# Optimization experiments

Measured on AMD Instinct MI355X. Metric: run time of the kernel, lower is better.

The kernel has to match this reference:

```python
import jax, jax.numpy as jnp
import numpy as np

# Faithful JAX reference for VoxelModule.forward.
# The torch module builds, per batch element, a dict mapping
#   key = vx*10000 + vy*100 + vz  (vx,vy,vz = int(coord * (voxel_size-1)))
# to the list of point indices falling in that voxel.
# Dicts are not jit-able; the equivalent parallel/sort-based grouping is:
#   keys        [B,N] : per-point voxel key (same integer math as torch)
#   order       [B,N] : stable argsort of keys -> point indices grouped by voxel
#   sorted_keys [B,N] : keys in grouped order (run boundaries delimit voxels)
# This (keys, order, sorted_keys) triple encodes exactly the same grouping
# information as the list-of-dicts output.

B = 16
N = 500_000
VOXEL_SIZE = 40  # keys require per-axis index < 100, so voxel_size <= 100


def setup_inputs() -> dict:
    key = jax.random.key(0)
    point_cloud = jax.random.uniform(key, (B, N, 3), dtype=jnp.float32)  # coords in [0,1)
    return {"point_cloud": point_cloud, "voxel_size": VOXEL_SIZE}


def reference(point_cloud, voxel_size):
    # int(x) in Python truncates toward zero; coords are non-negative so
    # truncation == floor. astype(int32) truncates, matching torch code.
    idx = (point_cloud * (voxel_size - 1)).astype(jnp.int32)  # [B,N,3]
    keys = idx[..., 0] * 10000 + idx[..., 1] * 100 + idx[..., 2]  # [B,N]
    # Stable sort: within a voxel, point indices stay in ascending order,
    # matching the append order of the torch dict-building loop.
    order = jnp.argsort(keys, axis=-1, stable=True)  # [B,N] grouped point ids
    sorted_keys = jnp.take_along_axis(keys, order, axis=-1)  # [B,N]
    return keys, order, sorted_keys
```

## Files before the change

### kernel.cpp

```cpp
#include <hip/hip_runtime.h>


#define B 16
#define N 500000
#define BN (B * N)
#define NC2 122
#define RELB 512
#define CAP2 4736
#define TPB1 256
#define NW1 (TPB1 / 64)
#define PPB 2048
#define CPB ((N + PPB - 1) / PPB)
#define NIT4 3

__global__ __launch_bounds__(TPB1, 8) void pass1(const float* __restrict__ pc,
                                                 const int* __restrict__ vs,
                                                 int* __restrict__ keys,
                                                 int* __restrict__ ccnt,
                                                 int* __restrict__ staged) {
    int b = blockIdx.x / CPB;
    int chunk = blockIdx.x % CPB;
    int t = threadIdx.x;
    int w = t >> 6;
    int lane = t & 63;
    __shared__ int lh[NW1][NC2];
    __shared__ int lst[NC2];
    __shared__ int gadj[NC2];
    __shared__ int lim[NC2];
    __shared__ int buf[PPB];
    __shared__ unsigned char cidb[PPB];
    for (int k = lane; k < NC2; k += 64) lh[w][k] = 0;
    float scale = (float)(vs[0] - 1);
    long gb0 = (long)b * N;
    int i0 = chunk * PPB + t * 8;
    int c2v[8], rv[8], pk8[8];
    bool valid = (i0 < N);
    if (valid) {
        const float4* F = (const float4*)(pc + 3 * (gb0 + i0));
        float4 f0 = F[0], f1 = F[1], f2 = F[2], f3 = F[3], f4 = F[4], f5 = F[5];
        float xs[8] = {f0.x, f0.w, f1.z, f2.y, f3.x, f3.w, f4.z, f5.y};
        float ys[8] = {f0.y, f1.x, f1.w, f2.z, f3.y, f4.x, f4.w, f5.z};
        float zs[8] = {f0.z, f1.y, f2.x, f2.w, f3.z, f4.y, f5.x, f5.w};
        int kk[8];
#pragma unroll
        for (int j = 0; j < 8; ++j) {
            int vx = (int)(xs[j] * scale);
            int vy = (int)(ys[j] * scale);
            int vz = (int)(zs[j] * scale);
            kk[j] = vx * 10000 + vy * 100 + vz;
            int lin = (vx * 40 + vy) * 40 + vz;
            int c2 = lin >> 9;
            c2v[j] = c2;
            pk8[j] = ((lin & 511) << 19) | (i0 + j);
            rv[j] = atomicAdd(&lh[w][c2], 1);
        }
        int4 k0; k0.x = kk[0]; k0.y = kk[1]; k0.z = kk[2]; k0.w = kk[3];
        int4 k1; k1.x = kk[4]; k1.y = kk[5]; k1.z = kk[6]; k1.w = kk[7];
        int4* K = (int4*)(keys + gb0 + i0);
        K[0] = k0; K[1] = k1;
    }
    __syncthreads();
    if (t < 64) {
        int idx0 = 2 * t, idx1 = 2 * t + 1;
        int run0 = 0, run1 = 0;
        if (idx0 < NC2) {
#pragma unroll
            for (int ww = 0; ww < NW1; ++ww) { int v = lh[ww][idx0]; lh[ww][idx0] = run0; run0 += v; }
#pragma unroll
            for (int ww = 0; ww < NW1; ++ww) { int v = lh[ww][idx1]; lh[ww][idx1] = run1; run1 += v; }
        }
        int s = run0 + run1;
        int x = s;
#pragma unroll
        for (int d = 1; d < 64; d <<= 1) { int y = __shfl_up(x, d, 64); if (t >= d) x += y; }
        int excl = x - s;
        if (idx0 < NC2) {
            int l0 = excl, l1 = excl + run0;
            lst[idx0] = l0; lst[idx1] = l1;
            int g0 = run0 ? atomicAdd(&ccnt[b * NC2 + idx0], run0) : 0;
            int g1 = run1 ? atomicAdd(&ccnt[b * NC2 + idx1], run1) : 0;
            gadj[idx0] = idx0 * CAP2 + g0 - l0;
            gadj[idx1] = idx1 * CAP2 + g1 - l1;
            lim[idx0] = l0 + CAP2 - g0;
            lim[idx1] = l1 + CAP2 - g1;
        }
    }
    __syncthreads();
    if (valid) {
#pragma unroll
        for (int j = 0; j < 8; ++j) {
            int c2 = c2v[j];
            int pos = lst[c2] + lh[w][c2] + rv[j];
            buf[pos] = pk8[j];
            cidb[pos] = (unsigned char)c2;
        }
    }
    __syncthreads();
    int nval = N - chunk * PPB; if (nval > PPB) nval = PPB;
    long sbase = (long)b * NC2 * CAP2;
#pragma unroll
    for (int q = 0; q < PPB / TPB1; ++q) {
        int p = t + q * TPB1;
        if (p < nval) {
            int e = buf[p];
            int c = cidb[p];
            if (p < lim[c]) staged[sbase + gadj[c] + p] = e;
        }
    }
}

__global__ __launch_bounds__(512) void pass2(const int* __restrict__ ccnt,
                                             const int* __restrict__ staged,
                                             int* __restrict__ order_out,
                                             int* __restrict__ skeys_out) {
    int bc = blockIdx.x;
    int b = bc / NC2;
    int c2 = bc % NC2;
    int t = threadIdx.x;
    __shared__ int h[RELB];
    __shared__ int st[RELB + 1];
    __shared__ int skeyL[RELB];
    __shared__ int srt[CAP2];
    __shared__ int bsh;
    int cnt = ccnt[bc]; if (cnt > CAP2) cnt = CAP2;
    if (cnt == 0) return;

    {
        int z = t;
        h[z] = 0;
        int lin = (c2 << 9) + z;
        int vx = lin / 1600;
        int r = lin - vx * 1600;
        int vy = r / 40;
        int vz = r - vy * 40;
        skeyL[z] = vx * 10000 + vy * 100 + vz;
    }
    if (t < 64) {
        int idx0 = 2 * t, idx1 = 2 * t + 1;
        int v0 = 0, v1 = 0;
        if (idx0 < NC2) {
            v0 = ccnt[b * NC2 + idx0]; if (v0 > CAP2) v0 = CAP2;
            v1 = ccnt[b * NC2 + idx1]; if (v1 > CAP2) v1 = CAP2;
        }
        int s = v0 + v1;
        int x = s;
#pragma unroll
        for (int d = 1; d < 64; d <<= 1) { int y = __shfl_up(x, d, 64); if (t >= d) x += y; }
        int excl = x - s;
        if (idx0 == c2) bsh = excl;
        if (idx1 == c2) bsh = excl + v0;
    }
    __syncthreads();

    long rb = (long)bc * CAP2;
    const int4* reg4 = (const int4*)(staged + rb);
    int n4 = cnt >> 2;
    int4 ev4[NIT4];
#pragma unroll
    for (int q = 0; q < NIT4; ++q) {
        int p4 = t + q * 512;
        if (p4 < n4) {
            int4 e = reg4[p4];
            ev4[q] = e;
            atomicAdd(&h[e.x >> 19], 1);
            atomicAdd(&h[e.y >> 19], 1);
            atomicAdd(&h[e.z >> 19], 1);
            atomicAdd(&h[e.w >> 19], 1);
        }
    }
    int evt = 0; bool tv = false;
    {
        int p = (n4 << 2) + t;
        if (p < cnt) { evt = staged[rb + p]; tv = true; atomicAdd(&h[evt >> 19], 1); }
    }
    __syncthreads();

    if (t < 64) {
        int vals[8]; int s = 0;
#pragma unroll
        for (int j = 0; j < 8; ++j) { int v = h[8 * t + j]; vals[j] = s; s += v; }
        int x = s;
#pragma unroll
        for (int d = 1; d < 64; d <<= 1) { int y = __shfl_up(x, d, 64); if (t >= d) x += y; }
        int excl = x - s;
#pragma unroll
        for (int j = 0; j < 8; ++j) { st[8 * t + j] = excl + vals[j]; h[8 * t + j] = 0; }
        if (t == 63) st[RELB] = x;
    }
    __syncthreads();

#pragma unroll
    for (int q = 0; q < NIT4; ++q) {
        int p4 = t + q * 512;
        if (p4 < n4) {
            int4 e = ev4[q];
            int z0 = e.x >> 19; srt[st[z0] + atomicAdd(&h[z0], 1)] = e.x;
            int z1 = e.y >> 19; srt[st[z1] + atomicAdd(&h[z1], 1)] = e.y;
            int z2 = e.z >> 19; srt[st[z2] + atomicAdd(&h[z2], 1)] = e.z;
            int z3 = e.w >> 19; srt[st[z3] + atomicAdd(&h[z3], 1)] = e.w;
        }
    }
    if (tv) { int z = evt >> 19; srt[st[z] + atomicAdd(&h[z], 1)] = evt; }
    __syncthreads();

    long ob = (long)b * N + bsh;
    for (int p = t; p < cnt; p += 512) {
        int v = srt[p];
        int z = v >> 19;
        int s = st[z], e2 = st[z + 1];
        int rank = 0;
        for (int j = s; j < e2; ++j) rank += (srt[j] < v);
        order_out[ob + s + rank] = v & 0x7FFFF;
        skeys_out[ob + s + rank] = skeyL[z];
    }
}

extern "C" void kernel_launch(void* const* d_in, const int* in_sizes, int n_in,
                              void* d_out, int out_size, void* d_ws, size_t ws_size,
                              hipStream_t stream) {
    const float* pc = (const float*)d_in[0];
    const int* vs = (const int*)d_in[1];
    int* out = (int*)d_out;
    int* keys_out = out;
    int* order_out = out + BN;
    int* skeys_out = out + 2 * BN;

    int* ccnt = (int*)d_ws;
    int* staged = ccnt + B * NC2;

    hipMemsetAsync(ccnt, 0, (size_t)B * NC2 * sizeof(int), stream);
    pass1<<<B * CPB, TPB1, 0, stream>>>(pc, vs, keys_out, ccnt, staged);
    pass2<<<B * NC2, 512, 0, stream>>>(ccnt, staged, order_out, skeys_out);
}
```

Measured before the change: 231.9 us.

## Enlarge pass1 chunks to 8192 points, 16 per thread, nontemporal key stores

Pass1 now runs 512 threads per block, each handling 16 points, so every block bins 8192 points instead of 2048. Larger chunks cut the number of per-block global atomics on the coarse-bucket counters and give longer contiguous scatter runs into the staged buffer. Per-point bucket id and local rank are packed into one register to save registers, and key writes use nontemporal vector stores. The trade-offs are more shared memory and registers per block, fewer resident blocks, and a longer serial scan across 8 warps.

```diff
diff --git a/kernel.cpp b/kernel.cpp
--- a/kernel.cpp
+++ b/kernel.cpp
@@ -7,17 +7,20 @@
 #define NC2 122
 #define RELB 512
 #define CAP2 4736
-#define TPB1 256
+#define TPB1 512
 #define NW1 (TPB1 / 64)
-#define PPB 2048
+#define PPB 8192
+#define PPT 16
 #define CPB ((N + PPB - 1) / PPB)
 #define NIT4 3
 
-__global__ __launch_bounds__(TPB1, 8) void pass1(const float* __restrict__ pc,
-                                                 const int* __restrict__ vs,
-                                                 int* __restrict__ keys,
-                                                 int* __restrict__ ccnt,
-                                                 int* __restrict__ staged) {
+typedef int vint4 __attribute__((ext_vector_type(4)));
+
+__global__ __launch_bounds__(TPB1) void pass1(const float* __restrict__ pc,
+                                              const int* __restrict__ vs,
+                                              int* __restrict__ keys,
+                                              int* __restrict__ ccnt,
+                                              int* __restrict__ staged) {
     int b = blockIdx.x / CPB;
     int chunk = blockIdx.x % CPB;
     int t = threadIdx.x;
@@ -32,32 +35,34 @@
     for (int k = lane; k < NC2; k += 64) lh[w][k] = 0;
     float scale = (float)(vs[0] - 1);
     long gb0 = (long)b * N;
-    int i0 = chunk * PPB + t * 8;
-    int c2v[8], rv[8], pk8[8];
+    int i0 = chunk * PPB + t * PPT;
+    int pr[PPT];
+    int pk[PPT];
     bool valid = (i0 < N);
     if (valid) {
         const float4* F = (const float4*)(pc + 3 * (gb0 + i0));
-        float4 f0 = F[0], f1 = F[1], f2 = F[2], f3 = F[3], f4 = F[4], f5 = F[5];
-        float xs[8] = {f0.x, f0.w, f1.z, f2.y, f3.x, f3.w, f4.z, f5.y};
-        float ys[8] = {f0.y, f1.x, f1.w, f2.z, f3.y, f4.x, f4.w, f5.z};
-        float zs[8] = {f0.z, f1.y, f2.x, f2.w, f3.z, f4.y, f5.x, f5.w};
-        int kk[8];
-#pragma unroll
-        for (int j = 0; j < 8; ++j) {
-            int vx = (int)(xs[j] * scale);
-            int vy = (int)(ys[j] * scale);
-            int vz = (int)(zs[j] * scale);
-            kk[j] = vx * 10000 + vy * 100 + vz;
-            int lin = (vx * 40 + vy) * 40 + vz;
-            int c2 = lin >> 9;
-            c2v[j] = c2;
-            pk8[j] = ((lin & 511) << 19) | (i0 + j);
-            rv[j] = atomicAdd(&lh[w][c2], 1);
-        }
-        int4 k0; k0.x = kk[0]; k0.y = kk[1]; k0.z = kk[2]; k0.w = kk[3];
-        int4 k1; k1.x = kk[4]; k1.y = kk[5]; k1.z = kk[6]; k1.w = kk[7];
-        int4* K = (int4*)(keys + gb0 + i0);
-        K[0] = k0; K[1] = k1;
+#pragma unroll
+        for (int g = 0; g < 4; ++g) {
+            float4 f0 = F[3 * g], f1 = F[3 * g + 1], f2 = F[3 * g + 2];
+            float xs[4] = {f0.x, f0.w, f1.z, f2.y};
+            float ys[4] = {f0.y, f1.x, f1.w, f2.z};
+            float zs[4] = {f0.z, f1.y, f2.x, f2.w};
+            int kk[4];
+#pragma unroll
+            for (int j = 0; j < 4; ++j) {
+                int vx = (int)(xs[j] * scale);
+                int vy = (int)(ys[j] * scale);
+                int vz = (int)(zs[j] * scale);
+                kk[j] = vx * 10000 + vy * 100 + vz;
+                int lin = (vx * 40 + vy) * 40 + vz;
+                int c2 = lin >> 9;
+                int rv = atomicAdd(&lh[w][c2], 1);
+                pr[4 * g + j] = (c2 << 13) | rv;
+                pk[4 * g + j] = ((lin & 511) << 19) | (i0 + 4 * g + j);
+            }
+            vint4 kv; kv.x = kk[0]; kv.y = kk[1]; kv.z = kk[2]; kv.w = kk[3];
+            __builtin_nontemporal_store(kv, (vint4*)(keys + gb0 + i0) + g);
+        }
     }
     __syncthreads();
     if (t < 64) {
@@ -88,10 +93,11 @@
     __syncthreads();
     if (valid) {
 #pragma unroll
-        for (int j = 0; j < 8; ++j) {
-            int c2 = c2v[j];
-            int pos = lst[c2] + lh[w][c2] + rv[j];
-            buf[pos] = pk8[j];
+        for (int j = 0; j < PPT; ++j) {
+            int c2 = pr[j] >> 13;
+            int rv = pr[j] & 8191;
+            int pos = lst[c2] + lh[w][c2] + rv;
+            buf[pos] = pk[j];
             cidb[pos] = (unsigned char)c2;
         }
     }
@@ -228,7 +234,7 @@
     int* ccnt = (int*)d_ws;
     int* staged = ccnt + B * NC2;
 
-    hipMemsetAsync(ccnt, 0, (size_t)B * NC2 * sizeof(int), stream);
+    (void)hipMemsetAsync(ccnt, 0, (size_t)B * NC2 * sizeof(int), stream);
     pass1<<<B * CPB, TPB1, 0, stream>>>(pc, vs, keys_out, ccnt, staged);
     pass2<<<B * NC2, 512, 0, stream>>>(ccnt, staged, order_out, skeys_out);
 }
```

After: 261.7 us. +12.9%, slower.
